# Performance work log

Hardware: AMD Instinct MI355X
Metric: run time of the kernel (lower is better)

## Reference

```python
import jax, jax.numpy as jnp
import numpy as np

BETA = 0.25


def setup_inputs() -> dict:
    key = jax.random.key(0)
    k1, k2 = jax.random.split(key)
    ze = jax.random.normal(k1, (16, 64, 64, 64), dtype=jnp.float32)  # (B, L, H, W)
    # codebook init mirrors uniform_(-1/K, 1/K)
    K = 1024
    emb = jax.random.uniform(k2, (K, 64), dtype=jnp.float32, minval=-1.0 / K, maxval=1.0 / K)
    return {"ze": ze, "emb": emb}


def reference(ze, emb):
    B, L, H, W = ze.shape
    K = emb.shape[0]
    # (B, H, W, L) -> (N, L)
    zf = jnp.transpose(ze, (0, 2, 3, 1)).reshape(-1, L)
    # squared euclidean distances (N, K)
    d = (jnp.sum(zf * zf, axis=1, keepdims=True)
         + jnp.sum(emb * emb, axis=1)
         - 2.0 * zf @ emb.T)
    idx = jnp.argmin(d, axis=1)  # (N,)
    # direct gather == one-hot @ emb
    z_q = jnp.transpose(emb[idx].reshape(B, H, W, L), (0, 3, 1, 2))
    loss = (jnp.mean((jax.lax.stop_gradient(z_q) - ze) ** 2)
            + BETA * jnp.mean((z_q - jax.lax.stop_gradient(ze)) ** 2))
    # straight-through estimator
    z_q_st = ze + jax.lax.stop_gradient(z_q - ze)
    # perplexity of code usage
    counts = jnp.zeros((K,), dtype=zf.dtype).at[idx].add(1.0)
    e_mean = counts / zf.shape[0]
    perplexity = jnp.exp(-jnp.sum(e_mean * jnp.log(e_mean + 1e-10)))
    return z_q_st, loss, idx.reshape(-1, 1)
```

## Files before the change

kernel.cpp:

```cpp
#include <hip/hip_runtime.h>

typedef short bf16x8 __attribute__((ext_vector_type(8)));
typedef float f32x4  __attribute__((ext_vector_type(4)));

#define CAP 12

#define WS_LOSS 0
#define WS_EBF  64

#define L_EBF   0
#define L_ZBF   131072
#define L_MARG  147456
#define L_CCNT  147968
#define L_CSLOT 148480
#define L_TOTAL 154624

__device__ __forceinline__ unsigned short f2bf(float f) {
    unsigned u = __float_as_uint(f);
    return (unsigned short)((u + 0x7fffu + ((u >> 16) & 1u)) >> 16);
}

__device__ __forceinline__ float np_pairwise_sumsq64(const float* a) {
    float r[8];
    #pragma unroll
    for (int j = 0; j < 8; ++j) r[j] = __fmul_rn(a[j], a[j]);
    #pragma unroll
    for (int i = 8; i < 64; i += 8)
        #pragma unroll
        for (int j = 0; j < 8; ++j)
            r[j] = __fadd_rn(r[j], __fmul_rn(a[i + j], a[i + j]));
    return __fadd_rn(
        __fadd_rn(__fadd_rn(r[0], r[1]), __fadd_rn(r[2], r[3])),
        __fadd_rn(__fadd_rn(r[4], r[5]), __fadd_rn(r[6], r[7])));
}

__global__ __launch_bounds__(256) void prep_kernel(
    const float* __restrict__ emb, unsigned short* __restrict__ ebf,
    float* __restrict__ loss)
{
    int k = blockIdx.x * 256 + threadIdx.x;
    if (k == 0) *loss = 0.0f;
    if (k < 1024) {
        float e[64];
        #pragma unroll
        for (int l = 0; l < 64; ++l) e[l] = emb[k * 64 + l];
        int tile = k >> 4, r = k & 15;
        #pragma unroll
        for (int j = 0; j < 8; ++j) {
            bf16x8 v;
            #pragma unroll
            for (int m = 0; m < 8; ++m) v[m] = (short)f2bf(e[j * 8 + m]);
            *(bf16x8*)(ebf + tile * 1024 + j * 128 + r * 8) = v;
        }
    }
}

__global__ __launch_bounds__(256, 1) void vq_kernel(
    const float* __restrict__ ze, const float* __restrict__ emb,
    const unsigned short* __restrict__ ebf,
    float* __restrict__ out_zq, float* __restrict__ out_idxf,
    float* __restrict__ loss)
{
    extern __shared__ char smem[];
    unsigned short* ebf_l = (unsigned short*)(smem + L_EBF);
    unsigned short* zbf   = (unsigned short*)(smem + L_ZBF);
    float*          marg_l = (float*)(smem + L_MARG);
    int*            ccnt   = (int*)(smem + L_CCNT);
    int*            cslot  = (int*)(smem + L_CSLOT);

    const int t = threadIdx.x;
    const int n0 = blockIdx.x * 128;
    const int gbase = (n0 >> 12) * 262144 + (n0 & 4095);

    float z[64];
    float znorm = 0.0f;

    if (t < 128) {
        const float* zp = ze + gbase + t;
        #pragma unroll
        for (int l = 0; l < 64; ++l) z[l] = zp[l * 4096];
        ccnt[t] = 0;
        znorm = np_pairwise_sumsq64(z);
        float S = 0.0f;
        #pragma unroll
        for (int l = 0; l < 64; ++l) S += fabsf(z[l]);
        marg_l[t] = 1.67e-5f * S + 2.0e-4f;
        const int sw = t & 7;
        #pragma unroll
        for (int c = 0; c < 8; ++c) {
            bf16x8 bv;
            #pragma unroll
            for (int m = 0; m < 8; ++m) bv[m] = (short)f2bf(z[c * 8 + m]);
            *(bf16x8*)&zbf[t * 64 + ((c ^ sw) * 8)] = bv;
        }
    } else {
        const int tt = t - 128;
        #pragma unroll 8
        for (int it = 0; it < 64; ++it) {
            int off = it * 1024 + tt * 8;
            *(bf16x8*)&ebf_l[off] = *(const bf16x8*)&ebf[off];
        }
    }
    __syncthreads();

    const int wv = t >> 6;
    const int lane = t & 63;
    const int r = lane & 15;
    const int q = lane >> 4;
    const int wp = wv * 32;
    const int p0 = wp + r, p1 = wp + 16 + r;
    const int sw = r & 7;

    bf16x8 a00 = *(bf16x8*)&zbf[p0 * 64 + ((q       ^ sw) * 8)];
    bf16x8 a01 = *(bf16x8*)&zbf[p0 * 64 + (((q + 4) ^ sw) * 8)];
    bf16x8 a10 = *(bf16x8*)&zbf[p1 * 64 + ((q       ^ sw) * 8)];
    bf16x8 a11 = *(bf16x8*)&zbf[p1 * 64 + (((q + 4) ^ sw) * 8)];
    const unsigned short* bptr = ebf_l + q * 128 + r * 8;

    float rm[8];
    #pragma unroll
    for (int i = 0; i < 8; ++i) rm[i] = 1e30f;
    #pragma unroll 4
    for (int tile = 0; tile < 64; ++tile) {
        bf16x8 b0 = *(const bf16x8*)(bptr + tile * 1024);
        bf16x8 b1 = *(const bf16x8*)(bptr + tile * 1024 + 512);
        f32x4 c0 = {0.f, 0.f, 0.f, 0.f}, c1 = {0.f, 0.f, 0.f, 0.f};
        c0 = __builtin_amdgcn_mfma_f32_16x16x32_bf16(a00, b0, c0, 0, 0, 0);
        c0 = __builtin_amdgcn_mfma_f32_16x16x32_bf16(a01, b1, c0, 0, 0, 0);
        c1 = __builtin_amdgcn_mfma_f32_16x16x32_bf16(a10, b0, c1, 0, 0, 0);
        c1 = __builtin_amdgcn_mfma_f32_16x16x32_bf16(a11, b1, c1, 0, 0, 0);
        #pragma unroll
        for (int i = 0; i < 4; ++i) {
            rm[i]     = fminf(rm[i],     c0[i] * -2.0f);
            rm[4 + i] = fminf(rm[4 + i], c1[i] * -2.0f);
        }
    }
    float thr[8];
    #pragma unroll
    for (int i = 0; i < 8; ++i) {
        float v = rm[i];
        v = fminf(v, __shfl_xor(v, 1, 16));
        v = fminf(v, __shfl_xor(v, 2, 16));
        v = fminf(v, __shfl_xor(v, 4, 16));
        v = fminf(v, __shfl_xor(v, 8, 16));
        int row = wp + ((i >= 4) ? 16 : 0) + q * 4 + (i & 3);
        thr[i] = v + marg_l[row];
    }

    #pragma unroll 4
    for (int tile = 0; tile < 64; ++tile) {
        bf16x8 b0 = *(const bf16x8*)(bptr + tile * 1024);
        bf16x8 b1 = *(const bf16x8*)(bptr + tile * 1024 + 512);
        f32x4 c0 = {0.f, 0.f, 0.f, 0.f}, c1 = {0.f, 0.f, 0.f, 0.f};
        c0 = __builtin_amdgcn_mfma_f32_16x16x32_bf16(a00, b0, c0, 0, 0, 0);
        c0 = __builtin_amdgcn_mfma_f32_16x16x32_bf16(a01, b1, c0, 0, 0, 0);
        c1 = __builtin_amdgcn_mfma_f32_16x16x32_bf16(a10, b0, c1, 0, 0, 0);
        c1 = __builtin_amdgcn_mfma_f32_16x16x32_bf16(a11, b1, c1, 0, 0, 0);
        int code = tile * 16 + r;
        #pragma unroll
        for (int i = 0; i < 4; ++i) {
            if (c0[i] * -2.0f <= thr[i]) {
                int pp = wp + q * 4 + i;
                int ci = atomicAdd(&ccnt[pp], 1);
                if (ci < CAP) cslot[pp * CAP + ci] = code;
            }
            if (c1[i] * -2.0f <= thr[4 + i]) {
                int pp = wp + 16 + q * 4 + i;
                int ci = atomicAdd(&ccnt[pp], 1);
                if (ci < CAP) cslot[pp * CAP + ci] = code;
            }
        }
    }
    __syncthreads();

    if (t < 128) {
        int cnt = ccnt[t]; if (cnt > CAP) cnt = CAP;
        float best = 1e30f; int bk = 1 << 20;
        for (int c = 0; c < cnt; ++c) {
            int k = cslot[t * CAP + c];
            float e[64];
            const float4* er = (const float4*)(emb + k * 64);
            #pragma unroll
            for (int j = 0; j < 16; ++j) {
                float4 v = er[j];
                e[4*j] = v.x; e[4*j+1] = v.y; e[4*j+2] = v.z; e[4*j+3] = v.w;
            }
            float en = np_pairwise_sumsq64(e);
            float acc = 0.0f;
            #pragma unroll
            for (int l = 0; l < 64; ++l) acc = fmaf(z[l], e[l], acc);
            float sc = __fsub_rn(__fadd_rn(znorm, en), __fmul_rn(2.0f, acc));
            if (sc < best || (sc == best && k < bk)) { best = sc; bk = k; }
        }
        out_idxf[n0 + t] = (float)bk;

        const float4* er = (const float4*)(emb + bk * 64);
        float ls = 0.0f;
        #pragma unroll
        for (int j = 0; j < 16; ++j) {
            float4 v = er[j];
            float vv[4] = {v.x, v.y, v.z, v.w};
            #pragma unroll
            for (int m = 0; m < 4; ++m) {
                int l = 4 * j + m;
                out_zq[gbase + t + l * 4096] = vv[m];
                float d = vv[m] - z[l];
                ls = fmaf(d, d, ls);
            }
        }
        #pragma unroll
        for (int off = 32; off > 0; off >>= 1) ls += __shfl_down(ls, off, 64);
        if ((t & 63) == 0) atomicAdd(loss, ls);
    }
}

__global__ void finalize_kernel(const float* __restrict__ loss, float* __restrict__ out_loss)
{
    *out_loss = 1.25f * (*loss) / 4194304.0f;
}

extern "C" void kernel_launch(void* const* d_in, const int* in_sizes, int n_in,
                              void* d_out, int out_size, void* d_ws, size_t ws_size,
                              hipStream_t stream)
{
    const float* ze  = (const float*)d_in[0];
    const float* emb = (const float*)d_in[1];
    float* out = (float*)d_out;
    float* out_zq   = out;
    float* out_loss = out + 4194304;
    float* out_idxf = out + 4194305;

    char* w = (char*)d_ws;
    float*          ws_loss = (float*)(w + WS_LOSS);
    unsigned short* ebf     = (unsigned short*)(w + WS_EBF);

    static bool attr_set = false;
    if (!attr_set) {
        hipFuncSetAttribute((const void*)vq_kernel,
                            hipFuncAttributeMaxDynamicSharedMemorySize, L_TOTAL);
        attr_set = true;
    }

    prep_kernel<<<4, 256, 0, stream>>>(emb, ebf, ws_loss);
    vq_kernel<<<512, 256, L_TOTAL, stream>>>(ze, emb, ebf, out_zq, out_idxf, ws_loss);
    finalize_kernel<<<1, 1, 0, stream>>>(ws_loss, out_loss);
}
```

Measured before the change: 157.0 us.

## Process 256 rows per block, alias z staging into codebook LDS, fuse finalize

Each block now handles 256 rows with all 256 threads loading z, up from 128 rows with half the threads copying the codebook. The bf16 z staging area is reused as codebook LDS after the A fragments move into registers. Each wave computes four 16-row groups per codebook tile, with B fragments double-buffered from LDS. The finalize kernel is replaced by a last-block-done atomic counter. The intent is better reuse of each B fragment, one fewer launch and half as many blocks (256 on 256 CUs), at the cost of more register pressure and a serialized load phase before the codebook copy.

```diff
diff --git a/kernel.cpp b/kernel.cpp
--- a/kernel.cpp
+++ b/kernel.cpp
@@ -6,14 +6,14 @@
 #define CAP 12
 
 #define WS_LOSS 0
+#define WS_DONE 8
 #define WS_EBF  64
 
 #define L_EBF   0
-#define L_ZBF   131072
-#define L_MARG  147456
-#define L_CCNT  147968
-#define L_CSLOT 148480
-#define L_TOTAL 154624
+#define L_MARG  131072
+#define L_CCNT  132096
+#define L_CSLOT 133120
+#define L_TOTAL 145408
 
 __device__ __forceinline__ unsigned short f2bf(float f) {
     unsigned u = __float_as_uint(f);
@@ -36,10 +36,10 @@
 
 __global__ __launch_bounds__(256) void prep_kernel(
     const float* __restrict__ emb, unsigned short* __restrict__ ebf,
-    float* __restrict__ loss)
+    float* __restrict__ loss, int* __restrict__ done)
 {
     int k = blockIdx.x * 256 + threadIdx.x;
-    if (k == 0) *loss = 0.0f;
+    if (k == 0) { *loss = 0.0f; *done = 0; }
     if (k < 1024) {
         float e[64];
         #pragma unroll
@@ -55,145 +55,165 @@
     }
 }
 
-__global__ __launch_bounds__(256, 1) void vq_kernel(
+__global__ __launch_bounds__(256)
+__attribute__((amdgpu_waves_per_eu(1, 1)))
+void vq_kernel(
     const float* __restrict__ ze, const float* __restrict__ emb,
     const unsigned short* __restrict__ ebf,
     float* __restrict__ out_zq, float* __restrict__ out_idxf,
-    float* __restrict__ loss)
+    float* __restrict__ loss, int* __restrict__ done,
+    float* __restrict__ out_loss)
 {
     extern __shared__ char smem[];
-    unsigned short* ebf_l = (unsigned short*)(smem + L_EBF);
-    unsigned short* zbf   = (unsigned short*)(smem + L_ZBF);
+    unsigned short* ebf_l  = (unsigned short*)(smem + L_EBF);
+    unsigned short* zbf    = (unsigned short*)(smem + L_EBF);
     float*          marg_l = (float*)(smem + L_MARG);
     int*            ccnt   = (int*)(smem + L_CCNT);
     int*            cslot  = (int*)(smem + L_CSLOT);
 
     const int t = threadIdx.x;
-    const int n0 = blockIdx.x * 128;
+    const int n0 = blockIdx.x * 256;
     const int gbase = (n0 >> 12) * 262144 + (n0 & 4095);
 
     float z[64];
-    float znorm = 0.0f;
-
-    if (t < 128) {
+    {
         const float* zp = ze + gbase + t;
         #pragma unroll
         for (int l = 0; l < 64; ++l) z[l] = zp[l * 4096];
-        ccnt[t] = 0;
-        znorm = np_pairwise_sumsq64(z);
+    }
+    ccnt[t] = 0;
+    const float znorm = np_pairwise_sumsq64(z);
+    {
         float S = 0.0f;
         #pragma unroll
         for (int l = 0; l < 64; ++l) S += fabsf(z[l]);
         marg_l[t] = 1.67e-5f * S + 2.0e-4f;
-        const int sw = t & 7;
+    }
+    {
+        const int swt = t & 7;
         #pragma unroll
         for (int c = 0; c < 8; ++c) {
             bf16x8 bv;
             #pragma unroll
             for (int m = 0; m < 8; ++m) bv[m] = (short)f2bf(z[c * 8 + m]);
-            *(bf16x8*)&zbf[t * 64 + ((c ^ sw) * 8)] = bv;
-        }
-    } else {
-        const int tt = t - 128;
+            *(bf16x8*)&zbf[t * 64 + ((c ^ swt) * 8)] = bv;
+        }
+    }
+    __syncthreads();
+
+    const int wv = t >> 6, lane = t & 63;
+    const int r = lane & 15, q = lane >> 4;
+    const int wp = wv * 64;
+    const int sw = r & 7;
+    bf16x8 a0[4], a1[4];
+    #pragma unroll
+    for (int rg = 0; rg < 4; ++rg) {
+        int pg = wp + rg * 16 + r;
+        a0[rg] = *(bf16x8*)&zbf[pg * 64 + ((q ^ sw) * 8)];
+        a1[rg] = *(bf16x8*)&zbf[pg * 64 + (((q + 4) ^ sw) * 8)];
+    }
+    __syncthreads();
+
+    {
+        const bf16x8* src = (const bf16x8*)ebf;
+        bf16x8* dst = (bf16x8*)ebf_l;
         #pragma unroll 8
-        for (int it = 0; it < 64; ++it) {
-            int off = it * 1024 + tt * 8;
-            *(bf16x8*)&ebf_l[off] = *(const bf16x8*)&ebf[off];
-        }
-    }
-    __syncthreads();
-
-    const int wv = t >> 6;
-    const int lane = t & 63;
-    const int r = lane & 15;
-    const int q = lane >> 4;
-    const int wp = wv * 32;
-    const int p0 = wp + r, p1 = wp + 16 + r;
-    const int sw = r & 7;
-
-    bf16x8 a00 = *(bf16x8*)&zbf[p0 * 64 + ((q       ^ sw) * 8)];
-    bf16x8 a01 = *(bf16x8*)&zbf[p0 * 64 + (((q + 4) ^ sw) * 8)];
-    bf16x8 a10 = *(bf16x8*)&zbf[p1 * 64 + ((q       ^ sw) * 8)];
-    bf16x8 a11 = *(bf16x8*)&zbf[p1 * 64 + (((q + 4) ^ sw) * 8)];
+        for (int i = 0; i < 32; ++i) dst[t + i * 256] = src[t + i * 256];
+    }
+    __syncthreads();
+
     const unsigned short* bptr = ebf_l + q * 128 + r * 8;
 
-    float rm[8];
-    #pragma unroll
-    for (int i = 0; i < 8; ++i) rm[i] = 1e30f;
-    #pragma unroll 4
-    for (int tile = 0; tile < 64; ++tile) {
-        bf16x8 b0 = *(const bf16x8*)(bptr + tile * 1024);
-        bf16x8 b1 = *(const bf16x8*)(bptr + tile * 1024 + 512);
-        f32x4 c0 = {0.f, 0.f, 0.f, 0.f}, c1 = {0.f, 0.f, 0.f, 0.f};
-        c0 = __builtin_amdgcn_mfma_f32_16x16x32_bf16(a00, b0, c0, 0, 0, 0);
-        c0 = __builtin_amdgcn_mfma_f32_16x16x32_bf16(a01, b1, c0, 0, 0, 0);
-        c1 = __builtin_amdgcn_mfma_f32_16x16x32_bf16(a10, b0, c1, 0, 0, 0);
-        c1 = __builtin_amdgcn_mfma_f32_16x16x32_bf16(a11, b1, c1, 0, 0, 0);
-        #pragma unroll
-        for (int i = 0; i < 4; ++i) {
-            rm[i]     = fminf(rm[i],     c0[i] * -2.0f);
-            rm[4 + i] = fminf(rm[4 + i], c1[i] * -2.0f);
-        }
-    }
-    float thr[8];
-    #pragma unroll
-    for (int i = 0; i < 8; ++i) {
-        float v = rm[i];
-        v = fminf(v, __shfl_xor(v, 1, 16));
-        v = fminf(v, __shfl_xor(v, 2, 16));
-        v = fminf(v, __shfl_xor(v, 4, 16));
-        v = fminf(v, __shfl_xor(v, 8, 16));
-        int row = wp + ((i >= 4) ? 16 : 0) + q * 4 + (i & 3);
-        thr[i] = v + marg_l[row];
-    }
-
-    #pragma unroll 4
-    for (int tile = 0; tile < 64; ++tile) {
-        bf16x8 b0 = *(const bf16x8*)(bptr + tile * 1024);
-        bf16x8 b1 = *(const bf16x8*)(bptr + tile * 1024 + 512);
-        f32x4 c0 = {0.f, 0.f, 0.f, 0.f}, c1 = {0.f, 0.f, 0.f, 0.f};
-        c0 = __builtin_amdgcn_mfma_f32_16x16x32_bf16(a00, b0, c0, 0, 0, 0);
-        c0 = __builtin_amdgcn_mfma_f32_16x16x32_bf16(a01, b1, c0, 0, 0, 0);
-        c1 = __builtin_amdgcn_mfma_f32_16x16x32_bf16(a10, b0, c1, 0, 0, 0);
-        c1 = __builtin_amdgcn_mfma_f32_16x16x32_bf16(a11, b1, c1, 0, 0, 0);
-        int code = tile * 16 + r;
-        #pragma unroll
-        for (int i = 0; i < 4; ++i) {
-            if (c0[i] * -2.0f <= thr[i]) {
-                int pp = wp + q * 4 + i;
-                int ci = atomicAdd(&ccnt[pp], 1);
-                if (ci < CAP) cslot[pp * CAP + ci] = code;
+    float rm[16];
+    #pragma unroll
+    for (int i = 0; i < 16; ++i) rm[i] = -1e30f;
+    {
+        bf16x8 pb0[2], pb1[2];
+        pb0[0] = *(const bf16x8*)(bptr);
+        pb1[0] = *(const bf16x8*)(bptr + 512);
+        pb0[1] = *(const bf16x8*)(bptr + 1024);
+        pb1[1] = *(const bf16x8*)(bptr + 1536);
+        #pragma unroll 4
+        for (int tile = 0; tile < 64; ++tile) {
+            bf16x8 b0 = pb0[tile & 1], b1 = pb1[tile & 1];
+            int nt = tile + 2; if (nt > 63) nt = 63;
+            pb0[tile & 1] = *(const bf16x8*)(bptr + nt * 1024);
+            pb1[tile & 1] = *(const bf16x8*)(bptr + nt * 1024 + 512);
+            #pragma unroll
+            for (int rg = 0; rg < 4; ++rg) {
+                f32x4 c = {0.f, 0.f, 0.f, 0.f};
+                c = __builtin_amdgcn_mfma_f32_16x16x32_bf16(a0[rg], b0, c, 0, 0, 0);
+                c = __builtin_amdgcn_mfma_f32_16x16x32_bf16(a1[rg], b1, c, 0, 0, 0);
+                #pragma unroll
+                for (int i = 0; i < 4; ++i)
+                    rm[rg * 4 + i] = fmaxf(rm[rg * 4 + i], c[i]);
             }
-            if (c1[i] * -2.0f <= thr[4 + i]) {
-                int pp = wp + 16 + q * 4 + i;
-                int ci = atomicAdd(&ccnt[pp], 1);
-                if (ci < CAP) cslot[pp * CAP + ci] = code;
+        }
+    }
+    float thr[16];
+    #pragma unroll
+    for (int j = 0; j < 16; ++j) {
+        float v = rm[j];
+        v = fmaxf(v, __shfl_xor(v, 1, 16));
+        v = fmaxf(v, __shfl_xor(v, 2, 16));
+        v = fmaxf(v, __shfl_xor(v, 4, 16));
+        v = fmaxf(v, __shfl_xor(v, 8, 16));
+        int row = wp + (j >> 2) * 16 + q * 4 + (j & 3);
+        thr[j] = v - 0.5f * marg_l[row];
+    }
+
+    {
+        bf16x8 pb0[2], pb1[2];
+        pb0[0] = *(const bf16x8*)(bptr);
+        pb1[0] = *(const bf16x8*)(bptr + 512);
+        pb0[1] = *(const bf16x8*)(bptr + 1024);
+        pb1[1] = *(const bf16x8*)(bptr + 1536);
+        #pragma unroll 4
+        for (int tile = 0; tile < 64; ++tile) {
+            bf16x8 b0 = pb0[tile & 1], b1 = pb1[tile & 1];
+            int nt = tile + 2; if (nt > 63) nt = 63;
+            pb0[tile & 1] = *(const bf16x8*)(bptr + nt * 1024);
+            pb1[tile & 1] = *(const bf16x8*)(bptr + nt * 1024 + 512);
+            int code = tile * 16 + r;
+            #pragma unroll
+            for (int rg = 0; rg < 4; ++rg) {
+                f32x4 c = {0.f, 0.f, 0.f, 0.f};
+                c = __builtin_amdgcn_mfma_f32_16x16x32_bf16(a0[rg], b0, c, 0, 0, 0);
+                c = __builtin_amdgcn_mfma_f32_16x16x32_bf16(a1[rg], b1, c, 0, 0, 0);
+                #pragma unroll
+                for (int i = 0; i < 4; ++i) {
+                    if (c[i] >= thr[rg * 4 + i]) {
+                        int pp = wp + rg * 16 + q * 4 + i;
+                        int ci = atomicAdd(&ccnt[pp], 1);
+                        if (ci < CAP) cslot[pp * CAP + ci] = code;
+                    }
+                }
             }
         }
     }
     __syncthreads();
 
-    if (t < 128) {
-        int cnt = ccnt[t]; if (cnt > CAP) cnt = CAP;
-        float best = 1e30f; int bk = 1 << 20;
-        for (int c = 0; c < cnt; ++c) {
-            int k = cslot[t * CAP + c];
-            float e[64];
-            const float4* er = (const float4*)(emb + k * 64);
-            #pragma unroll
-            for (int j = 0; j < 16; ++j) {
-                float4 v = er[j];
-                e[4*j] = v.x; e[4*j+1] = v.y; e[4*j+2] = v.z; e[4*j+3] = v.w;
-            }
-            float en = np_pairwise_sumsq64(e);
-            float acc = 0.0f;
-            #pragma unroll
-            for (int l = 0; l < 64; ++l) acc = fmaf(z[l], e[l], acc);
-            float sc = __fsub_rn(__fadd_rn(znorm, en), __fmul_rn(2.0f, acc));
-            if (sc < best || (sc == best && k < bk)) { best = sc; bk = k; }
-        }
-        out_idxf[n0 + t] = (float)bk;
-
+    int cnt = ccnt[t]; if (cnt > CAP) cnt = CAP;
+    float best = 1e30f; int bk = 1 << 20;
+    for (int c = 0; c < cnt; ++c) {
+        int k = cslot[t * CAP + c];
+        float e[64];
+        const float4* er = (const float4*)(emb + k * 64);
+        #pragma unroll
+        for (int j = 0; j < 16; ++j) {
+            float4 v = er[j];
+            e[4*j] = v.x; e[4*j+1] = v.y; e[4*j+2] = v.z; e[4*j+3] = v.w;
+        }
+        float en = np_pairwise_sumsq64(e);
+        float acc = 0.0f;
+        #pragma unroll
+        for (int l = 0; l < 64; ++l) acc = fmaf(z[l], e[l], acc);
+        float sc = __fsub_rn(__fadd_rn(znorm, en), __fmul_rn(2.0f, acc));
+        if (sc < best || (sc == best && k < bk)) { best = sc; bk = k; }
+    }
+    out_idxf[n0 + t] = (float)bk;
+
+    {
         const float4* er = (const float4*)(emb + bk * 64);
         float ls = 0.0f;
         #pragma unroll
@@ -210,13 +230,19 @@
         }
         #pragma unroll
         for (int off = 32; off > 0; off >>= 1) ls += __shfl_down(ls, off, 64);
-        if ((t & 63) == 0) atomicAdd(loss, ls);
-    }
-}
-
-__global__ void finalize_kernel(const float* __restrict__ loss, float* __restrict__ out_loss)
-{
-    *out_loss = 1.25f * (*loss) / 4194304.0f;
+        if (lane == 0) atomicAdd(loss, ls);
+    }
+
+    __syncthreads();
+    if (t == 0) {
+        __threadfence();
+        int old = atomicAdd(done, 1);
+        if (old == (int)gridDim.x - 1) {
+            __threadfence();
+            float total = atomicAdd(loss, 0.0f);
+            *out_loss = 1.25f * total / 4194304.0f;
+        }
+    }
 }
 
 extern "C" void kernel_launch(void* const* d_in, const int* in_sizes, int n_in,
@@ -232,6 +258,7 @@
 
     char* w = (char*)d_ws;
     float*          ws_loss = (float*)(w + WS_LOSS);
+    int*            ws_done = (int*)(w + WS_DONE);
     unsigned short* ebf     = (unsigned short*)(w + WS_EBF);
 
     static bool attr_set = false;
@@ -241,7 +268,7 @@
         attr_set = true;
     }
 
-    prep_kernel<<<4, 256, 0, stream>>>(emb, ebf, ws_loss);
-    vq_kernel<<<512, 256, L_TOTAL, stream>>>(ze, emb, ebf, out_zq, out_idxf, ws_loss);
-    finalize_kernel<<<1, 1, 0, stream>>>(ws_loss, out_loss);
-}
+    prep_kernel<<<4, 256, 0, stream>>>(emb, ebf, ws_loss, ws_done);
+    vq_kernel<<<256, 256, L_TOTAL, stream>>>(ze, emb, ebf, out_zq, out_idxf,
+                                             ws_loss, ws_done, out_loss);
+}
```

Result: faster. 141.5 us (-9.9%).
